# Optimization experiments

Measured on AMD Instinct MI355X. Metric: run time of the kernel, lower is better.

The kernel has to match this reference:

```python
import jax, jax.numpy as jnp
import numpy as np

M, NQ, NKV, DX, DT = 8, 1024, 1024, 512, 2
H, HD = 8, 64            # num_heads, head_dim
INNER = H * HD           # 512
KHID = 16                # kernel MLP hidden dim
SCALE = HD ** -0.5


def setup_inputs() -> dict:
    key = jax.random.key(0)
    ks = jax.random.split(key, 16)
    s = lambda fan_in: 1.0 / np.sqrt(fan_in)
    return {
        "xq": jax.random.normal(ks[0], (M, NQ, DX), jnp.float32),
        "xk": jax.random.normal(ks[1], (M, NKV, DX), jnp.float32),
        "xv": jax.random.normal(ks[2], (M, NKV, DX), jnp.float32),
        "tq": jax.random.normal(ks[3], (M, NQ, DT), jnp.float32),
        "tk": jax.random.normal(ks[4], (M, NKV, DT), jnp.float32),
        # attention projections (bias=False for q/k/v, Linear bias for out)
        "w_q": jax.random.normal(ks[5], (DX, INNER), jnp.float32) * s(DX),
        "w_k": jax.random.normal(ks[6], (DX, INNER), jnp.float32) * s(DX),
        "w_v": jax.random.normal(ks[7], (DX, INNER), jnp.float32) * s(DX),
        "w_out": jax.random.normal(ks[8], (INNER, DX), jnp.float32) * s(INNER),
        "b_out": jnp.zeros((DX,), jnp.float32),
        # kernel MLP: dt -> KHID -> H (per-head pairwise bias)
        "kw1": jax.random.normal(ks[9], (DT, KHID), jnp.float32) * s(DT),
        "kb1": jnp.zeros((KHID,), jnp.float32),
        "kw2": jax.random.normal(ks[10], (KHID, H), jnp.float32) * s(KHID),
        "kb2": jnp.zeros((H,), jnp.float32),
    }


def reference(xq, xk, xv, tq, tk, w_q, w_k, w_v, w_out, b_out, kw1, kb1, kw2, kb2):
    # pairwise differences of input locations: [m, nq, nkv, dt]
    diff = tq[:, :, None, :] - tk[:, None, :, :]
    # kernel MLP -> per-head bias, rearranged to [m, h, nq, nkv]
    hmid = jax.nn.relu(diff @ kw1 + kb1)          # [m, nq, nkv, KHID]
    dots = jnp.einsum('mqkc,ch->mhqk', hmid, kw2) + kb2[None, :, None, None]
    # token attention: standard scaled QK scores
    q = (xq @ w_q).reshape(M, NQ, H, HD)          # [m, nq, h, d]
    k = (xk @ w_k).reshape(M, NKV, H, HD)
    token_dots = jnp.einsum('mqhd,mkhd->mhqk', q, k) * SCALE
    dots = dots + token_dots
    attn = jax.nn.softmax(dots, axis=-1)          # softmax over keys
    v = (xv @ w_v).reshape(M, NKV, H, HD)
    out = jnp.einsum('mhqk,mkhd->mqhd', attn, v).reshape(M, NQ, INNER)
    return out @ w_out + b_out                    # [m, nq, dx]
```

## Files before the change

### kernel.cpp

```cpp
#include <hip/hip_runtime.h>


typedef unsigned short u16;
typedef unsigned int   u32;
typedef short bf8 __attribute__((ext_vector_type(8)));
typedef float f4  __attribute__((ext_vector_type(4)));

#define Mb 8
#define SCALE 0.125f

__device__ __forceinline__ u16 f2bf(float f) {
    union { float f; u32 u; } v; v.f = f;
    u32 r = v.u + 0x7fffu + ((v.u >> 16) & 1u);
    return (u16)(r >> 16);
}
__device__ __forceinline__ u32 pk2(float a, float b) {
    return (u32)f2bf(a) | ((u32)f2bf(b) << 16);
}

struct GArgs {
    const void*  A[3];
    const float* W[3];
    void*        C[3];
    const float* bias;
    int          modeT[3];
    int          outf32;
    int          abf16;
};

__global__ __launch_bounds__(256) void gemm_mfma(GArgs g) {
    __shared__ u16 Xs[4][128][8];
    __shared__ u16 Ws[4][128][8];

    const int z   = blockIdx.z;
    const int tid = threadIdx.x;
    const int w = tid >> 6, lane = tid & 63, quad = lane >> 4, l16 = lane & 15;
    const int wm = w >> 1, wn = w & 1;
    const int n0 = blockIdx.x * 128, t0 = blockIdx.y * 128;
    const int trans = g.modeT[z];

    f4 acc[4][4];
    #pragma unroll
    for (int i = 0; i < 4; ++i)
        #pragma unroll
        for (int j = 0; j < 4; ++j) acc[i][j] = (f4)0.f;

    const float* Wp = g.W[z];

    for (int kc = 0; kc < 512; kc += 32) {
        __syncthreads();
        {
            const int row = tid >> 1, half = tid & 1;
            if (g.abf16) {
                const u16* ap = (const u16*)g.A[z] + (size_t)(t0 + row) * 512 + kc + half * 16;
                uint4 v0 = *(const uint4*)ap;
                uint4 v1 = *(const uint4*)(ap + 8);
                *(uint4*)&Xs[half * 2][row][0]     = v0;
                *(uint4*)&Xs[half * 2 + 1][row][0] = v1;
            } else {
                const float* ap = (const float*)g.A[z] + (size_t)(t0 + row) * 512 + kc + half * 16;
                float4 a0 = *(const float4*)(ap + 0);
                float4 a1 = *(const float4*)(ap + 4);
                float4 a2 = *(const float4*)(ap + 8);
                float4 a3 = *(const float4*)(ap + 12);
                uint4 v0, v1;
                v0.x = pk2(a0.x, a0.y); v0.y = pk2(a0.z, a0.w);
                v0.z = pk2(a1.x, a1.y); v0.w = pk2(a1.z, a1.w);
                v1.x = pk2(a2.x, a2.y); v1.y = pk2(a2.z, a2.w);
                v1.z = pk2(a3.x, a3.y); v1.w = pk2(a3.z, a3.w);
                *(uint4*)&Xs[half * 2][row][0]     = v0;
                *(uint4*)&Xs[half * 2 + 1][row][0] = v1;
            }
        }
        #pragma unroll
        for (int i = 0; i < 4; ++i) {
            const int s = tid + i * 256;
            const int n = s & 127, kg = s >> 7;
            const int kb = kc + kg * 4;
            float v0 = Wp[(size_t)(kb + 0) * 512 + n0 + n];
            float v1 = Wp[(size_t)(kb + 1) * 512 + n0 + n];
            float v2 = Wp[(size_t)(kb + 2) * 512 + n0 + n];
            float v3 = Wp[(size_t)(kb + 3) * 512 + n0 + n];
            uint2 pw; pw.x = pk2(v0, v1); pw.y = pk2(v2, v3);
            *(uint2*)&Ws[kg >> 1][n][(kg & 1) * 4] = pw;
        }
        __syncthreads();

        const u16 (*Aop)[128][8] = trans ? Xs : Ws;
        const u16 (*Bop)[128][8] = trans ? Ws : Xs;
        const int arow = (trans ? wm : wn) * 64;
        const int brow = (trans ? wn : wm) * 64;
        bf8 af[4], bf[4];
        #pragma unroll
        for (int i = 0; i < 4; ++i) af[i] = *(const bf8*)&Aop[quad][arow + i * 16 + l16][0];
        #pragma unroll
        for (int j = 0; j < 4; ++j) bf[j] = *(const bf8*)&Bop[quad][brow + j * 16 + l16][0];
        #pragma unroll
        for (int i = 0; i < 4; ++i)
            #pragma unroll
            for (int j = 0; j < 4; ++j)
                acc[i][j] = __builtin_amdgcn_mfma_f32_16x16x32_bf16(af[i], bf[j], acc[i][j], 0, 0, 0);
    }

    if (g.outf32) {
        float* Co = (float*)g.C[z];
        #pragma unroll
        for (int i = 0; i < 4; ++i) {
            const int nb = n0 + wn * 64 + i * 16 + quad * 4;
            float4 bv = *(const float4*)&g.bias[nb];
            #pragma unroll
            for (int j = 0; j < 4; ++j) {
                const int tok = t0 + wm * 64 + j * 16 + l16;
                float4 st;
                st.x = acc[i][j][0] + bv.x; st.y = acc[i][j][1] + bv.y;
                st.z = acc[i][j][2] + bv.z; st.w = acc[i][j][3] + bv.w;
                *(float4*)&Co[(size_t)tok * 512 + nb] = st;
            }
        }
    } else if (!trans) {
        u16* C = (u16*)g.C[z];
        #pragma unroll
        for (int i = 0; i < 4; ++i) {
            const int nb = n0 + wn * 64 + i * 16 + quad * 4;
            #pragma unroll
            for (int j = 0; j < 4; ++j) {
                const int tok = t0 + wm * 64 + j * 16 + l16;
                uint2 pw;
                pw.x = pk2(acc[i][j][0], acc[i][j][1]);
                pw.y = pk2(acc[i][j][2], acc[i][j][3]);
                *(uint2*)&C[(size_t)tok * 512 + nb] = pw;
            }
        }
    } else {
        u16* Vt = (u16*)g.C[z];
        #pragma unroll
        for (int i = 0; i < 4; ++i) {
            const int tokb = t0 + wm * 64 + i * 16 + quad * 4;
            const int mb = tokb >> 10, tb = tokb & 1023;
            #pragma unroll
            for (int j = 0; j < 4; ++j) {
                const int n = n0 + wn * 64 + j * 16 + l16;
                uint2 pw;
                pw.x = pk2(acc[i][j][0], acc[i][j][1]);
                pw.y = pk2(acc[i][j][2], acc[i][j][3]);
                *(uint2*)&Vt[(size_t)mb * 524288 + (size_t)n * 1024 + tb] = pw;
            }
        }
    }
}

__global__ __launch_bounds__(256) void attn_mfma(
    const u16* __restrict__ Q, const u16* __restrict__ K,
    const u16* __restrict__ Vt,
    const float* __restrict__ tqp, const float* __restrict__ tkp,
    const float* __restrict__ kw1, const float* __restrict__ kb1,
    const float* __restrict__ kw2,
    u16* __restrict__ O)
{
    __shared__ u16   sK[8][64][8];
    __shared__ u16   sV[8][64][8];
    __shared__ float sv[16][68];
    __shared__ u16   sP[4][16][68];

    const int tid = threadIdx.x;
    const int w = tid >> 6, lane = tid & 63, quad = lane >> 4, l16 = lane & 15;
    const int qt = blockIdx.x, h = blockIdx.y, m = blockIdx.z;
    const int q0 = qt * 64;
    const size_t qtok = (size_t)m * 1024 + q0 + w * 16 + l16;

    bf8 qf[2];
    {
        const u16* qp = Q + qtok * 512 + h * 64 + quad * 8;
        qf[0] = *(const bf8*)qp;
        qf[1] = *(const bf8*)(qp + 32);
    }
    float u[16], w2h[16];
    {
        const float t0v = tqp[qtok * 2], t1v = tqp[qtok * 2 + 1];
        #pragma unroll
        for (int c = 0; c < 16; ++c) {
            u[c] = fmaf(t0v, kw1[c], fmaf(t1v, kw1[16 + c], kb1[c]));
            w2h[c] = kw2[c * 8 + h];
        }
    }

    float mrun = -1e30f, lrun = 0.f;
    f4 o[4];
    #pragma unroll
    for (int d = 0; d < 4; ++d) o[d] = (f4)0.f;

    for (int kt = 0; kt < 16; ++kt) {
        const int k0 = kt * 64;
        __syncthreads();
        #pragma unroll
        for (int i = 0; i < 2; ++i) {
            const int s = tid + i * 256;
            const int seg = s >> 6, key = s & 63;
            const u16* kp = K + ((size_t)m * 1024 + k0 + key) * 512 + h * 64 + seg * 8;
            *(uint4*)&sK[seg][key][0] = *(const uint4*)kp;
        }
        #pragma unroll
        for (int i = 0; i < 2; ++i) {
            const int s = tid + i * 256;
            const int ks = s >> 6, d = s & 63;
            const u16* vp = Vt + (size_t)m * 524288 + (size_t)(h * 64 + d) * 1024 + k0 + ks * 8;
            *(uint4*)&sV[ks][d][0] = *(const uint4*)vp;
        }
        {
            const int c = tid >> 4, k4 = (tid & 15) * 4;
            const float* tkq = tkp + ((size_t)m * 1024 + k0 + k4) * 2;
            float4 ta = *(const float4*)tkq;
            float4 tb = *(const float4*)(tkq + 4);
            const float w0 = kw1[c], w1 = kw1[16 + c];
            float4 vv;
            vv.x = fmaf(ta.x, w0, ta.y * w1);
            vv.y = fmaf(ta.z, w0, ta.w * w1);
            vv.z = fmaf(tb.x, w0, tb.y * w1);
            vv.w = fmaf(tb.z, w0, tb.w * w1);
            *(float4*)&sv[c][k4] = vv;
        }
        __syncthreads();

        f4 s[4];
        #pragma unroll
        for (int msub = 0; msub < 4; ++msub) {
            bf8 kf0 = *(const bf8*)&sK[quad][msub * 16 + l16][0];
            bf8 kf1 = *(const bf8*)&sK[4 + quad][msub * 16 + l16][0];
            s[msub] = __builtin_amdgcn_mfma_f32_16x16x32_bf16(kf0, qf[0], (f4)0.f, 0, 0, 0);
            s[msub] = __builtin_amdgcn_mfma_f32_16x16x32_bf16(kf1, qf[1], s[msub], 0, 0, 0);
        }
        #pragma unroll
        for (int msub = 0; msub < 4; ++msub) {
            const int kb = msub * 16 + quad * 4;
            f4 b = (f4)0.f;
            #pragma unroll
            for (int c = 0; c < 16; ++c) {
                float4 vv = *(const float4*)&sv[c][kb];
                const float uc = u[c], wc = w2h[c];
                b[0] = fmaf(fmaxf(uc - vv.x, 0.f), wc, b[0]);
                b[1] = fmaf(fmaxf(uc - vv.y, 0.f), wc, b[1]);
                b[2] = fmaf(fmaxf(uc - vv.z, 0.f), wc, b[2]);
                b[3] = fmaf(fmaxf(uc - vv.w, 0.f), wc, b[3]);
            }
            s[msub] = s[msub] * SCALE + b;
        }
        float mx = -1e30f;
        #pragma unroll
        for (int msub = 0; msub < 4; ++msub) {
            mx = fmaxf(mx, fmaxf(fmaxf(s[msub][0], s[msub][1]),
                                 fmaxf(s[msub][2], s[msub][3])));
        }
        mx = fmaxf(mx, __shfl_xor(mx, 16));
        mx = fmaxf(mx, __shfl_xor(mx, 32));
        const float mnew = fmaxf(mrun, mx);
        const float alpha = __expf(mrun - mnew);
        float ps = 0.f;
        #pragma unroll
        for (int msub = 0; msub < 4; ++msub) {
            #pragma unroll
            for (int r = 0; r < 4; ++r) {
                float p = __expf(s[msub][r] - mnew);
                s[msub][r] = p;
                ps += p;
            }
        }
        ps += __shfl_xor(ps, 16);
        ps += __shfl_xor(ps, 32);
        lrun = lrun * alpha + ps;
        mrun = mnew;
        #pragma unroll
        for (int d = 0; d < 4; ++d) o[d] = o[d] * alpha;
        #pragma unroll
        for (int msub = 0; msub < 4; ++msub) {
            uint2 pw;
            pw.x = pk2(s[msub][0], s[msub][1]);
            pw.y = pk2(s[msub][2], s[msub][3]);
            *(uint2*)&sP[w][l16][msub * 16 + quad * 4] = pw;
        }
        #pragma unroll
        for (int dsub = 0; dsub < 4; ++dsub) {
            #pragma unroll
            for (int kc2 = 0; kc2 < 2; ++kc2) {
                bf8 vf = *(const bf8*)&sV[kc2 * 4 + quad][dsub * 16 + l16][0];
                bf8 pf = *(const bf8*)&sP[w][l16][kc2 * 32 + quad * 8];
                o[dsub] = __builtin_amdgcn_mfma_f32_16x16x32_bf16(vf, pf, o[dsub], 0, 0, 0);
            }
        }
    }

    const float inv = 1.f / lrun;
    #pragma unroll
    for (int dsub = 0; dsub < 4; ++dsub) {
        uint2 pw;
        pw.x = pk2(o[dsub][0] * inv, o[dsub][1] * inv);
        pw.y = pk2(o[dsub][2] * inv, o[dsub][3] * inv);
        *(uint2*)&O[qtok * 512 + h * 64 + dsub * 16 + quad * 4] = pw;
    }
}

extern "C" void kernel_launch(void* const* d_in, const int* in_sizes, int n_in,
                              void* d_out, int out_size, void* d_ws, size_t ws_size,
                              hipStream_t stream) {
    const float* xq    = (const float*)d_in[0];
    const float* xk    = (const float*)d_in[1];
    const float* xv    = (const float*)d_in[2];
    const float* tq    = (const float*)d_in[3];
    const float* tk    = (const float*)d_in[4];
    const float* w_q   = (const float*)d_in[5];
    const float* w_k   = (const float*)d_in[6];
    const float* w_v   = (const float*)d_in[7];
    const float* w_out = (const float*)d_in[8];
    const float* b_out = (const float*)d_in[9];
    const float* kw1   = (const float*)d_in[10];
    const float* kb1   = (const float*)d_in[11];
    const float* kw2   = (const float*)d_in[12];

    const size_t nTok = (size_t)Mb * 1024 * 512;
    u16* Q  = (u16*)d_ws;
    u16* Kp = Q + nTok;
    u16* Vt = Kp + nTok;
    u16* O  = Vt + nTok;

    GArgs gq;
    gq.A[0] = xq;  gq.A[1] = xk;  gq.A[2] = xv;
    gq.W[0] = w_q; gq.W[1] = w_k; gq.W[2] = w_v;
    gq.C[0] = Q;   gq.C[1] = Kp;  gq.C[2] = Vt;
    gq.bias = nullptr;
    gq.modeT[0] = 0; gq.modeT[1] = 0; gq.modeT[2] = 1;
    gq.outf32 = 0; gq.abf16 = 0;
    gemm_mfma<<<dim3(4, 64, 3), 256, 0, stream>>>(gq);

    attn_mfma<<<dim3(16, 8, Mb), 256, 0, stream>>>(Q, Kp, Vt, tq, tk,
                                                   kw1, kb1, kw2, O);

    GArgs go;
    go.A[0] = O;     go.A[1] = O;     go.A[2] = O;
    go.W[0] = w_out; go.W[1] = w_out; go.W[2] = w_out;
    go.C[0] = d_out; go.C[1] = d_out; go.C[2] = d_out;
    go.bias = b_out;
    go.modeT[0] = 0; go.modeT[1] = 0; go.modeT[2] = 0;
    go.outf32 = 1; go.abf16 = 1;
    gemm_mfma<<<dim3(4, 64, 1), 256, 0, stream>>>(go);
}
```

Before: 307.4 us.

## Pre-convert activations and weights to bf16 in a separate prep kernel

Adds a prep kernel that converts xq/xk/xv to bf16 and transposes and converts the four weight matrices to bf16 (n-major) in workspace. The GEMM kernel then loads only bf16 with vectorized 16-byte loads for both operands, instead of converting fp32 on the fly and doing strided scalar weight loads. The goal is to cut GEMM load traffic and per-tile conversion work. The cost is an extra launch plus a full read/write pass over the activations (about 50 MB of traffic), which may outweigh the savings.

```diff
diff --git a/kernel.cpp b/kernel.cpp
--- a/kernel.cpp
+++ b/kernel.cpp
@@ -8,6 +8,7 @@
 
 #define Mb 8
 #define SCALE 0.125f
+#define NTOK 4194304
 
 __device__ __forceinline__ u16 f2bf(float f) {
     union { float f; u32 u; } v; v.f = f;
@@ -18,14 +19,64 @@
     return (u32)f2bf(a) | ((u32)f2bf(b) << 16);
 }
 
+struct PArgs {
+    const float* xs[3];
+    const float* ws[4];
+    u16* dstA;
+    u16* dstW;
+};
+
+__global__ __launch_bounds__(256) void prep(PArgs p) {
+    __shared__ u16 tl[64][80];
+    const int tid = threadIdx.x;
+    const int b = blockIdx.x;
+    if (b < 1536) {
+        #pragma unroll
+        for (int it = 0; it < 4; ++it) {
+            const u32 u = (u32)b * 256u + (u32)tid + (u32)it * 393216u;
+            const int arr = u >> 19;
+            const size_t off = (size_t)(u & 524287u) * 8;
+            const float* s = p.xs[arr];
+            float4 a0 = *(const float4*)(s + off);
+            float4 a1 = *(const float4*)(s + off + 4);
+            uint4 v;
+            v.x = pk2(a0.x, a0.y); v.y = pk2(a0.z, a0.w);
+            v.z = pk2(a1.x, a1.y); v.w = pk2(a1.z, a1.w);
+            *(uint4*)(p.dstA + (size_t)arr * NTOK + off) = v;
+        }
+    } else {
+        const int bb = b - 1536;
+        const int mat = bb >> 6, t = bb & 63;
+        const int kt = t >> 3, nt = t & 7;
+        const float* src = p.ws[mat] + (size_t)kt * 64 * 512 + (size_t)nt * 64;
+        const int r0 = tid >> 4, c4 = (tid & 15) * 4;
+        #pragma unroll
+        for (int rr = 0; rr < 4; ++rr) {
+            const int row = r0 + rr * 16;
+            float4 a = *(const float4*)(src + (size_t)row * 512 + c4);
+            tl[c4 + 0][row] = f2bf(a.x);
+            tl[c4 + 1][row] = f2bf(a.y);
+            tl[c4 + 2][row] = f2bf(a.z);
+            tl[c4 + 3][row] = f2bf(a.w);
+        }
+        __syncthreads();
+        u16* dst = p.dstW + (size_t)mat * 262144 + (size_t)nt * 64 * 512 + (size_t)kt * 64;
+        #pragma unroll
+        for (int i = 0; i < 2; ++i) {
+            const int s2 = tid + i * 256;
+            const int nrow = s2 >> 3, k8 = (s2 & 7) * 8;
+            *(uint4*)(dst + (size_t)nrow * 512 + k8) = *(const uint4*)&tl[nrow][k8];
+        }
+    }
+}
+
 struct GArgs {
-    const void*  A[3];
-    const float* W[3];
+    const u16*   A[3];
+    const u16*   W[3];
     void*        C[3];
     const float* bias;
     int          modeT[3];
     int          outf32;
-    int          abf16;
 };
 
 __global__ __launch_bounds__(256) void gemm_mfma(GArgs g) {
@@ -45,44 +96,25 @@
         #pragma unroll
         for (int j = 0; j < 4; ++j) acc[i][j] = (f4)0.f;
 
-    const float* Wp = g.W[z];
+    const u16* Ap = g.A[z];
+    const u16* Wp = g.W[z];
 
     for (int kc = 0; kc < 512; kc += 32) {
         __syncthreads();
         {
             const int row = tid >> 1, half = tid & 1;
-            if (g.abf16) {
-                const u16* ap = (const u16*)g.A[z] + (size_t)(t0 + row) * 512 + kc + half * 16;
-                uint4 v0 = *(const uint4*)ap;
-                uint4 v1 = *(const uint4*)(ap + 8);
-                *(uint4*)&Xs[half * 2][row][0]     = v0;
-                *(uint4*)&Xs[half * 2 + 1][row][0] = v1;
-            } else {
-                const float* ap = (const float*)g.A[z] + (size_t)(t0 + row) * 512 + kc + half * 16;
-                float4 a0 = *(const float4*)(ap + 0);
-                float4 a1 = *(const float4*)(ap + 4);
-                float4 a2 = *(const float4*)(ap + 8);
-                float4 a3 = *(const float4*)(ap + 12);
-                uint4 v0, v1;
-                v0.x = pk2(a0.x, a0.y); v0.y = pk2(a0.z, a0.w);
-                v0.z = pk2(a1.x, a1.y); v0.w = pk2(a1.z, a1.w);
-                v1.x = pk2(a2.x, a2.y); v1.y = pk2(a2.z, a2.w);
-                v1.z = pk2(a3.x, a3.y); v1.w = pk2(a3.z, a3.w);
-                *(uint4*)&Xs[half * 2][row][0]     = v0;
-                *(uint4*)&Xs[half * 2 + 1][row][0] = v1;
-            }
-        }
-        #pragma unroll
-        for (int i = 0; i < 4; ++i) {
+            const u16* ap = Ap + (size_t)(t0 + row) * 512 + kc + half * 16;
+            uint4 v0 = *(const uint4*)ap;
+            uint4 v1 = *(const uint4*)(ap + 8);
+            *(uint4*)&Xs[half * 2][row][0]     = v0;
+            *(uint4*)&Xs[half * 2 + 1][row][0] = v1;
+        }
+        #pragma unroll
+        for (int i = 0; i < 2; ++i) {
             const int s = tid + i * 256;
-            const int n = s & 127, kg = s >> 7;
-            const int kb = kc + kg * 4;
-            float v0 = Wp[(size_t)(kb + 0) * 512 + n0 + n];
-            float v1 = Wp[(size_t)(kb + 1) * 512 + n0 + n];
-            float v2 = Wp[(size_t)(kb + 2) * 512 + n0 + n];
-            float v3 = Wp[(size_t)(kb + 3) * 512 + n0 + n];
-            uint2 pw; pw.x = pk2(v0, v1); pw.y = pk2(v2, v3);
-            *(uint2*)&Ws[kg >> 1][n][(kg & 1) * 4] = pw;
+            const int seg = s & 3, n = s >> 2;
+            *(uint4*)&Ws[seg][n][0] =
+                *(const uint4*)(Wp + (size_t)(n0 + n) * 512 + kc + seg * 8);
         }
         __syncthreads();
 
@@ -315,30 +347,42 @@
     const float* kb1   = (const float*)d_in[11];
     const float* kw2   = (const float*)d_in[12];
 
-    const size_t nTok = (size_t)Mb * 1024 * 512;
     u16* Q  = (u16*)d_ws;
-    u16* Kp = Q + nTok;
-    u16* Vt = Kp + nTok;
-    u16* O  = Vt + nTok;
+    u16* Kp = Q  + NTOK;
+    u16* Vt = Kp + NTOK;
+    u16* Aq = Vt + NTOK;
+    u16* Ak = Aq + NTOK;
+    u16* Av = Ak + NTOK;
+    u16* Wq = Av + NTOK;
+    u16* Wk = Wq + 262144;
+    u16* Wv = Wk + 262144;
+    u16* Wo = Wv + 262144;
+    u16* O  = Aq;
+
+    PArgs p;
+    p.xs[0] = xq;  p.xs[1] = xk;  p.xs[2] = xv;
+    p.ws[0] = w_q; p.ws[1] = w_k; p.ws[2] = w_v; p.ws[3] = w_out;
+    p.dstA = Aq;   p.dstW = Wq;
+    prep<<<dim3(1792), 256, 0, stream>>>(p);
 
     GArgs gq;
-    gq.A[0] = xq;  gq.A[1] = xk;  gq.A[2] = xv;
-    gq.W[0] = w_q; gq.W[1] = w_k; gq.W[2] = w_v;
+    gq.A[0] = Aq;  gq.A[1] = Ak;  gq.A[2] = Av;
+    gq.W[0] = Wq;  gq.W[1] = Wk;  gq.W[2] = Wv;
     gq.C[0] = Q;   gq.C[1] = Kp;  gq.C[2] = Vt;
     gq.bias = nullptr;
     gq.modeT[0] = 0; gq.modeT[1] = 0; gq.modeT[2] = 1;
-    gq.outf32 = 0; gq.abf16 = 0;
+    gq.outf32 = 0;
     gemm_mfma<<<dim3(4, 64, 3), 256, 0, stream>>>(gq);
 
     attn_mfma<<<dim3(16, 8, Mb), 256, 0, stream>>>(Q, Kp, Vt, tq, tk,
                                                    kw1, kb1, kw2, O);
 
     GArgs go;
-    go.A[0] = O;     go.A[1] = O;     go.A[2] = O;
-    go.W[0] = w_out; go.W[1] = w_out; go.W[2] = w_out;
+    go.A[0] = O;   go.A[1] = O;   go.A[2] = O;
+    go.W[0] = Wo;  go.W[1] = Wo;  go.W[2] = Wo;
     go.C[0] = d_out; go.C[1] = d_out; go.C[2] = d_out;
     go.bias = b_out;
     go.modeT[0] = 0; go.modeT[1] = 0; go.modeT[2] = 0;
-    go.outf32 = 1; go.abf16 = 1;
+    go.outf32 = 1;
     gemm_mfma<<<dim3(4, 64, 1), 256, 0, stream>>>(go);
 }
```

Result: no change. 304.8 us (-0.9%).
